# Kernel optimization log

Hardware: AMD Instinct MI355X
Metric: run time of the kernel (lower is better)

Reference implementation:

```python
import jax, jax.numpy as jnp
import numpy as np

PATCH = 16      # sqrt(n_patches=256)
ALPHA = 10.0
HEADS, DH = 2, 64


def _fourier(coords, Bm):
    # coords: (HW, 2), Bm: (n_features, 2) -> (HW, 2*n_features)
    proj = 2.0 * jnp.pi * coords @ Bm.T
    return jnp.concatenate([jnp.cos(proj), jnp.sin(proj)], axis=-1)


def _forward(coords_decoding, tokens, B_q, B_l0, B_l1,
             qW, qb, toqW, tokvW, tooW, toob,
             bwW0, bwb0, bwW1, bwb1,
             modW0, modb0, modW1, modb1,
             hvW0, hvb0, outW0, outb0, outW1, outb1):
    B = coords_decoding.shape[0]
    Hh, Ww = coords_decoding.shape[1], coords_decoding.shape[2]
    coords = coords_decoding.reshape(B, -1, coords_decoding.shape[-1])
    grid = coords[0]                      # (HW, 2); coords_modulation is None -> same grid
    HW = grid.shape[0]
    m = tokens.shape[1]

    # patch indices and spatial bias
    row = jnp.clip((grid[:, 0] * PATCH).astype(jnp.int32), 0, PATCH - 1)
    col = jnp.clip((grid[:, 1] * PATCH).astype(jnp.int32), 0, PATCH - 1)
    idx = row * PATCH + col               # (HW,)
    t = idx.astype(jnp.float32) / (PATCH * PATCH)
    pos = (jnp.arange(m, dtype=jnp.float32) + 0.5) / m
    rel = -ALPHA * jnp.abs(t[None, :] - pos[:, None]) ** 2   # (m, HW)
    bias = rel.T                          # (HW, m), broadcast over batch & heads

    # query features (shared across batch)
    xq = jax.nn.relu(_fourier(grid, B_q) @ qW + qb)           # (HW, hd)
    xq_b = jnp.broadcast_to(xq[None], (B, HW, xq.shape[-1]))

    # cross attention with spatial bias
    q = (xq_b @ toqW).reshape(B, HW, HEADS, DH).transpose(0, 2, 1, 3)   # (B,h,HW,Dh)
    kv = tokens @ tokvW                                                  # (B,m,2*inner)
    k, v = jnp.split(kv, 2, axis=-1)
    k = k.reshape(B, m, HEADS, DH).transpose(0, 2, 1, 3)                 # (B,h,m,Dh)
    v = v.reshape(B, m, HEADS, DH).transpose(0, 2, 1, 3)
    sim = jnp.einsum('bhqd,bhkd->bhqk', q, k) * (DH ** -0.5) + bias[None, None]
    attn = jax.nn.softmax(sim, axis=-1)
    o = jnp.einsum('bhqk,bhkd->bhqd', attn, v)
    o = o.transpose(0, 2, 1, 3).reshape(B, HW, HEADS * DH)
    mod = o @ tooW + toob                                                # (B,HW,hd)

    # per-band MLP stack (layer_num = 2)
    def band(Bl, bwW, bwb, mW, mb):
        h = jax.nn.relu(_fourier(grid, Bl) @ bwW + bwb)                  # (HW,hd)
        return jax.nn.relu(h[None] + mod @ mW + mb)                      # (B,HW,hd)

    m0 = band(B_l0, bwW0, bwb0, modW0, modb0)
    m1 = band(B_l1, bwW1, bwb1, modW1, modb1)
    hv0 = m0
    hv1 = jax.nn.relu((m1 + hv0) @ hvW0 + hvb0)
    out = (hv0 @ outW0 + outb0) + (hv1 @ outW1 + outb1)                  # (B,HW,3)
    return out.reshape(B, Hh, Ww, -1)


def setup_inputs() -> dict:
    key = jax.random.key(0)
    ks = jax.random.split(key, 32)
    B, H, W, L = 4, 128, 128, 256
    fd, hd, cd, od = 64, 256, 256, 3
    nf = fd // 2
    inner = HEADS * DH

    def lin(k, i, o):
        return jax.random.normal(k, (i, o), dtype=jnp.float32) / np.sqrt(i).astype(np.float32)

    inp = {}
    inp['coords_decoding'] = jax.random.uniform(ks[0], (B, H, W, 2), dtype=jnp.float32)
    inp['tokens'] = jax.random.normal(ks[1], (B, L, cd), dtype=jnp.float32)
    inp['B_q'] = jax.random.normal(ks[2], (nf, 2), dtype=jnp.float32) / 16.0
    inp['B_l0'] = jax.random.normal(ks[3], (nf, 2), dtype=jnp.float32) / 128.0
    inp['B_l1'] = jax.random.normal(ks[4], (nf, 2), dtype=jnp.float32) / 32.0
    inp['qW'] = lin(ks[5], fd, hd); inp['qb'] = jnp.zeros((hd,), jnp.float32)
    inp['toqW'] = lin(ks[6], hd, inner)
    inp['tokvW'] = lin(ks[7], cd, inner * 2)
    inp['tooW'] = lin(ks[8], inner, hd); inp['toob'] = jnp.zeros((hd,), jnp.float32)
    inp['bwW0'] = lin(ks[9], fd, hd); inp['bwb0'] = jnp.zeros((hd,), jnp.float32)
    inp['bwW1'] = lin(ks[10], fd, hd); inp['bwb1'] = jnp.zeros((hd,), jnp.float32)
    inp['modW0'] = lin(ks[11], hd, hd); inp['modb0'] = jnp.zeros((hd,), jnp.float32)
    inp['modW1'] = lin(ks[12], hd, hd); inp['modb1'] = jnp.zeros((hd,), jnp.float32)
    inp['hvW0'] = lin(ks[13], hd, hd); inp['hvb0'] = jnp.zeros((hd,), jnp.float32)
    inp['outW0'] = lin(ks[14], hd, od); inp['outb0'] = jnp.zeros((od,), jnp.float32)
    inp['outW1'] = lin(ks[15], hd, od); inp['outb1'] = jnp.zeros((od,), jnp.float32)
    return inp


def reference(coords_decoding, tokens, B_q, B_l0, B_l1,
              qW, qb, toqW, tokvW, tooW, toob,
              bwW0, bwb0, bwW1, bwb1,
              modW0, modb0, modW1, modb1,
              hvW0, hvb0, outW0, outb0, outW1, outb1):
    return _forward(coords_decoding, tokens, B_q, B_l0, B_l1,
                    qW, qb, toqW, tokvW, tooW, toob,
                    bwW0, bwb0, bwW1, bwb1,
                    modW0, modb0, modW1, modb1,
                    hvW0, hvb0, outW0, outb0, outW1, outb1)
```

## Files before the change

### kernel.cpp

```cpp
#include <hip/hip_runtime.h>
#include <stdint.h>

constexpr int kHW = 16384;
constexpr int kB  = 4;
constexpr int kM  = 256;

typedef _Float16 half8 __attribute__((ext_vector_type(8)));
typedef __attribute__((ext_vector_type(4))) float f32x4;

__device__ __forceinline__ unsigned short f2h(float f) {
  _Float16 h = (_Float16)f;
  return __builtin_bit_cast(unsigned short, h);
}
__device__ __forceinline__ float h2f(unsigned short u) {
  return (float)__builtin_bit_cast(_Float16, u);
}
__device__ __forceinline__ int swz256(int row, int col) {
  int ch = col >> 3;
  ch = (ch & ~7) | ((ch ^ row) & 7);
  return row * 256 + ch * 8 + (col & 7);
}

__global__ __launch_bounds__(256) void wprep_kernel(
    const float* __restrict__ tooW, const float* __restrict__ modW0,
    const float* __restrict__ modW1, const float* __restrict__ hvW0,
    const float* __restrict__ qW, const float* __restrict__ bwW0,
    const float* __restrict__ bwW1, const float* __restrict__ toqW,
    unsigned short* __restrict__ tooWt, unsigned short* __restrict__ modW0t,
    unsigned short* __restrict__ modW1t, unsigned short* __restrict__ hvW0t,
    unsigned short* __restrict__ qWt, unsigned short* __restrict__ bw0t,
    unsigned short* __restrict__ bw1t, unsigned short* __restrict__ toqWt)
{
  int m = blockIdx.x, tid = threadIdx.x;
  const float* Ws[8] = {tooW, modW0, modW1, hvW0, qW, bwW0, bwW1, toqW};
  unsigned short* Wts[8] = {tooWt, modW0t, modW1t, hvW0t, qWt, bw0t, bw1t, toqWt};
  const int Ks[8] = {128, 256, 256, 256, 64, 64, 64, 256};
  const int Ns[8] = {256, 256, 256, 256, 256, 256, 256, 128};
  const float* W = Ws[m];
  unsigned short* Wt = Wts[m];
  int K = Ks[m], N = Ns[m];
  if (tid < N) {
    for (int kb = 0; kb < K / 8; kb++) {
      unsigned short sv[8];
#pragma unroll
      for (int i = 0; i < 8; i++)
        sv[i] = f2h(W[(kb * 8 + i) * N + tid]);
      *(uint4*)&Wt[tid * K + kb * 8] = *(const uint4*)sv;
    }
  }
}

__global__ __launch_bounds__(256) void kv_kernel(
    const float* __restrict__ tokens, const float* __restrict__ tokvW,
    unsigned short* __restrict__ kn_ws, unsigned short* __restrict__ vt_ws)
{
  __shared__ __align__(16) float tok[256];
  int b = blockIdx.y, j = blockIdx.x, c = threadIdx.x;
  tok[c] = tokens[(b * kM + j) * 256 + c];
  __syncthreads();
  float acc = 0.f;
  for (int i4 = 0; i4 < 64; i4++) {
    float4 t4 = *(const float4*)&tok[i4 * 4];
    acc += t4.x * tokvW[(i4*4+0)*256 + c] + t4.y * tokvW[(i4*4+1)*256 + c]
         + t4.z * tokvW[(i4*4+2)*256 + c] + t4.w * tokvW[(i4*4+3)*256 + c];
  }
  unsigned short hv = f2h(acc);
  if (c < 128) {
    int h = c >> 6, dd = c & 63;
    kn_ws[((size_t)(b*2+h)*256 + j) * 64 + dd] = hv;
  } else {
    int c2 = c - 128;
    int h = c2 >> 6, dd = c2 & 63;
    vt_ws[((size_t)(b*2+h)*64 + dd) * 256 + j] = hv;
  }
}

constexpr int kFPitch = 72;
constexpr int kXPitch = 264;

__global__ __launch_bounds__(256, 2) void feat_kernel(
    const float* __restrict__ coords,
    const float* __restrict__ Bq, const float* __restrict__ Bl0, const float* __restrict__ Bl1,
    const float* __restrict__ qb, const float* __restrict__ bwb0, const float* __restrict__ bwb1,
    const unsigned short* __restrict__ qWt, const unsigned short* __restrict__ bw0t,
    const unsigned short* __restrict__ bw1t, const unsigned short* __restrict__ toqWt,
    unsigned short* __restrict__ qc_ws,
    unsigned short* __restrict__ h0_hf, unsigned short* __restrict__ h1_hf)
{
  __shared__ __align__(16) unsigned short ff_s[3][32][kFPitch];
  __shared__ __align__(16) unsigned short xq_s[32][kXPitch];
  __shared__ float coords_s[64];

  int tid = threadIdx.x;
  int px0 = blockIdx.x * 32;
  int w = tid >> 6, ln = tid & 63;
  int c = ln & 15, q = ln >> 4;

  if (tid < 64) coords_s[tid] = coords[px0 * 2 + tid];
  __syncthreads();

#pragma unroll
  for (int r = 0; r < 24; r++) {
    int v = r * 256 + tid;
    int mat = v >> 11;
    int p = (v >> 6) & 31;
    int f = v & 63;
    int fr = f & 31;
    const float* Bm = (mat == 0) ? Bq : (mat == 1 ? Bl0 : Bl1);
    float x = coords_s[p * 2 + 0];
    float y = coords_s[p * 2 + 1];
    float proj = 6.283185307179586f * (x * Bm[fr*2+0] + y * Bm[fr*2+1]);
    float s, cc;
    __sincosf(proj, &s, &cc);
    ff_s[mat][p][f] = f2h((f < 32) ? cc : s);
  }
  __syncthreads();

  const f32x4 zero4 = {0.f, 0.f, 0.f, 0.f};

  for (int mat = 0; mat < 3; mat++) {
    const unsigned short* Wt = (mat == 0) ? qWt : (mat == 1 ? bw0t : bw1t);
    const float* bias = (mat == 0) ? qb : (mat == 1 ? bwb0 : bwb1);
    f32x4 acc[8];
#pragma unroll
    for (int i = 0; i < 8; i++) acc[i] = zero4;
#pragma unroll
    for (int ks = 0; ks < 2; ks++) {
      int koff = ks * 32 + q * 8;
      half8 bfr[4];
#pragma unroll
      for (int nt = 0; nt < 4; nt++)
        bfr[nt] = *(const half8*)(Wt + (size_t)(w*64 + nt*16 + c) * 64 + koff);
      half8 afr[2];
#pragma unroll
      for (int mt = 0; mt < 2; mt++)
        afr[mt] = *(const half8*)(&ff_s[mat][mt*16 + c][koff]);
#pragma unroll
      for (int mt = 0; mt < 2; mt++)
#pragma unroll
        for (int nt = 0; nt < 4; nt++)
          acc[mt*4+nt] = __builtin_amdgcn_mfma_f32_16x16x32_f16(afr[mt], bfr[nt], acc[mt*4+nt], 0, 0, 0);
    }
    float bv[4];
#pragma unroll
    for (int nt = 0; nt < 4; nt++) bv[nt] = bias[w*64 + nt*16 + c];
#pragma unroll
    for (int mt = 0; mt < 2; mt++)
#pragma unroll
      for (int nt = 0; nt < 4; nt++)
#pragma unroll
        for (int rg = 0; rg < 4; rg++) {
          int row = mt*16 + q*4 + rg, col = w*64 + nt*16 + c;
          unsigned short hv = f2h(fmaxf(acc[mt*4+nt][rg] + bv[nt], 0.f));
          if (mat == 0)      xq_s[row][col] = hv;
          else if (mat == 1) h0_hf[((size_t)(px0 + row)) * 256 + col] = hv;
          else               h1_hf[((size_t)(px0 + row)) * 256 + col] = hv;
        }
  }
  __syncthreads();

  {
    f32x4 acc2[4];
#pragma unroll
    for (int i = 0; i < 4; i++) acc2[i] = zero4;
#pragma unroll
    for (int kt = 0; kt < 8; kt++) {
      int koff = kt * 32 + q * 8;
      half8 bfr[2];
#pragma unroll
      for (int nt = 0; nt < 2; nt++)
        bfr[nt] = *(const half8*)(toqWt + (size_t)(w*32 + nt*16 + c) * 256 + koff);
      half8 afr[2];
#pragma unroll
      for (int mt = 0; mt < 2; mt++)
        afr[mt] = *(const half8*)(&xq_s[mt*16 + c][koff]);
#pragma unroll
      for (int mt = 0; mt < 2; mt++)
#pragma unroll
        for (int nt = 0; nt < 2; nt++)
          acc2[mt*2+nt] = __builtin_amdgcn_mfma_f32_16x16x32_f16(afr[mt], bfr[nt], acc2[mt*2+nt], 0, 0, 0);
    }
#pragma unroll
    for (int mt = 0; mt < 2; mt++)
#pragma unroll
      for (int nt = 0; nt < 2; nt++)
#pragma unroll
        for (int rg = 0; rg < 4; rg++) {
          int row = mt*16 + q*4 + rg, col = w*32 + nt*16 + c;
          qc_ws[((size_t)(px0 + row)) * 128 + col] = f2h(acc2[mt*2+nt][rg]);
        }
  }
}

__global__ __launch_bounds__(256, 2) void attn_kernel(
    const unsigned short* __restrict__ kn_ws,
    const unsigned short* __restrict__ vt_ws,
    const unsigned short* __restrict__ qc_ws,
    const float* __restrict__ coords,
    unsigned short* __restrict__ o_hf)
{
  __shared__ __align__(16) unsigned short P_s[64 * 256];

  int b = blockIdx.y;
  int px0 = blockIdx.x * 64;
  int tid = threadIdx.x;
  int w = tid >> 6, ln = tid & 63;
  int c = ln & 15, q = ln >> 4;

  float tv[4];
#pragma unroll
  for (int rg = 0; rg < 4; rg++) {
    int px = px0 + w*16 + q*4 + rg;
    float x = coords[px*2 + 0], y = coords[px*2 + 1];
    int r = min(max((int)(x * 16.0f), 0), 15);
    int cl = min(max((int)(y * 16.0f), 0), 15);
    tv[rg] = (float)(r * 16 + cl) * (1.0f / 256.0f);
  }

  const f32x4 zero4 = {0.f, 0.f, 0.f, 0.f};

  for (int h = 0; h < 2; h++) {
    f32x4 acc[16];
#pragma unroll
    for (int i = 0; i < 16; i++) acc[i] = zero4;
    const unsigned short* kbase = kn_ws + (size_t)(b*2+h) * 256 * 64;
    const unsigned short* qrow = qc_ws + (size_t)(px0 + w*16 + c) * 128 + h*64;
    half8 a0 = *(const half8*)(qrow + q*8);
    half8 a1 = *(const half8*)(qrow + 32 + q*8);
#pragma unroll
    for (int nt = 0; nt < 16; nt++) {
      const unsigned short* kr = kbase + (size_t)(nt*16 + c) * 64 + q*8;
      half8 b0 = *(const half8*)(kr);
      half8 b1 = *(const half8*)(kr + 32);
      acc[nt] = __builtin_amdgcn_mfma_f32_16x16x32_f16(a0, b0, acc[nt], 0, 0, 0);
      acc[nt] = __builtin_amdgcn_mfma_f32_16x16x32_f16(a1, b1, acc[nt], 0, 0, 0);
    }

    float lm[4];
#pragma unroll
    for (int rg = 0; rg < 4; rg++) {
      float mx = -1e30f;
#pragma unroll
      for (int nt = 0; nt < 16; nt++) {
        float pos = ((float)(nt*16 + c) + 0.5f) * (1.0f / 256.0f);
        float db = tv[rg] - pos;
        float sb = acc[nt][rg] * 0.125f - 10.0f * db * db;
        acc[nt][rg] = sb;
        mx = fmaxf(mx, sb);
      }
      lm[rg] = mx;
    }
#pragma unroll
    for (int s = 1; s < 16; s <<= 1)
#pragma unroll
      for (int rg = 0; rg < 4; rg++)
        lm[rg] = fmaxf(lm[rg], __shfl_xor(lm[rg], s, 64));

    float linv[4];
#pragma unroll
    for (int rg = 0; rg < 4; rg++) {
      float sum = 0.f;
      int row = w*16 + q*4 + rg;
#pragma unroll
      for (int nt = 0; nt < 16; nt++) {
        float e = __expf(acc[nt][rg] - lm[rg]);
        sum += e;
        P_s[swz256(row, nt*16 + c)] = f2h(e);
      }
      linv[rg] = sum;
    }
#pragma unroll
    for (int s = 1; s < 16; s <<= 1)
#pragma unroll
      for (int rg = 0; rg < 4; rg++)
        linv[rg] += __shfl_xor(linv[rg], s, 64);
#pragma unroll
    for (int rg = 0; rg < 4; rg++) linv[rg] = 1.0f / linv[rg];

    __syncthreads();

    f32x4 oacc[4];
#pragma unroll
    for (int i = 0; i < 4; i++) oacc[i] = zero4;
    const unsigned short* vbase = vt_ws + (size_t)(b*2+h) * 64 * 256;
#pragma unroll
    for (int kt = 0; kt < 8; kt++) {
      int koff = kt * 32 + q * 8;
      half8 af = *(const half8*)&P_s[swz256(w*16 + c, koff)];
#pragma unroll
      for (int nt = 0; nt < 4; nt++) {
        half8 bf = *(const half8*)(vbase + (size_t)(nt*16 + c) * 256 + koff);
        oacc[nt] = __builtin_amdgcn_mfma_f32_16x16x32_f16(af, bf, oacc[nt], 0, 0, 0);
      }
    }
#pragma unroll
    for (int nt = 0; nt < 4; nt++)
#pragma unroll
      for (int rg = 0; rg < 4; rg++) {
        int row = w*16 + q*4 + rg;
        o_hf[((size_t)(b * kHW + px0 + row)) * 128 + h*64 + nt*16 + c] =
            f2h(oacc[nt][rg] * linv[rg]);
      }
    __syncthreads();
  }
}

constexpr int kPitch = 264;

template <int KD>
__device__ __forceinline__ void gemm4(
    const unsigned short* abuf, const unsigned short* wt,
    f32x4* acc , int c, int q)
{
#pragma unroll
  for (int ks = 0; ks < KD / 32; ks++) {
    int koff = ks * 32 + q * 8;
    half8 bfr[4];
#pragma unroll
    for (int nt = 0; nt < 4; nt++)
      bfr[nt] = *(const half8*)(wt + (nt * 16 + c) * KD + koff);
    half8 afr[4];
#pragma unroll
    for (int mt = 0; mt < 4; mt++)
      afr[mt] = *(const half8*)(abuf + (mt * 16 + c) * kPitch + koff);
#pragma unroll
    for (int mt = 0; mt < 4; mt++)
#pragma unroll
      for (int nt = 0; nt < 4; nt++)
        acc[mt * 4 + nt] = __builtin_amdgcn_mfma_f32_16x16x32_f16(afr[mt], bfr[nt], acc[mt * 4 + nt], 0, 0, 0);
  }
}

__global__ __launch_bounds__(256, 2) void mlp_kernel(
    const unsigned short* __restrict__ o_hf,
    const unsigned short* __restrict__ h0_hf, const unsigned short* __restrict__ h1_hf,
    const unsigned short* __restrict__ tooWt, const float* __restrict__ toob,
    const unsigned short* __restrict__ modW0t, const float* __restrict__ modb0,
    const unsigned short* __restrict__ modW1t, const float* __restrict__ modb1,
    const unsigned short* __restrict__ hvW0t, const float* __restrict__ hvb0,
    const float* __restrict__ outW0, const float* __restrict__ outb0,
    const float* __restrict__ outW1, const float* __restrict__ outb1,
    float* __restrict__ dout)
{
  __shared__ __align__(16) unsigned short buf0[64 * kPitch];
  __shared__ __align__(16) unsigned short buf1[64 * kPitch];
  __shared__ __align__(16) unsigned short hbuf[16 * kPitch];
  __shared__ __align__(16) float scratch[64 * 3 * 4];

  int tid = threadIdx.x;
  int px0 = blockIdx.x * 16;
  int w = tid >> 6, ln = tid & 63;
  int c = ln & 15, q = ln >> 4;

#pragma unroll
  for (int i = 0; i < 4; i++) {
    int idx = i * 256 + tid;
    int r = idx >> 4, c8 = (idx & 15) * 8;
    int b = r >> 4, px = r & 15;
    uint4 v = *(const uint4*)(o_hf + ((size_t)(b * kHW + px0 + px)) * 128 + c8);
    *(uint4*)&buf0[r * kPitch + c8] = v;
  }
#pragma unroll
  for (int i = 0; i < 2; i++) {
    int idx = i * 256 + tid;
    int p = idx >> 5, c8 = (idx & 31) * 8;
    uint4 v = *(const uint4*)(h0_hf + ((size_t)(px0 + p)) * 256 + c8);
    *(uint4*)&hbuf[p * kPitch + c8] = v;
  }
  __syncthreads();

  f32x4 acc[16];
  const f32x4 zero4 = {0.f, 0.f, 0.f, 0.f};

#pragma unroll
  for (int i = 0; i < 16; i++) acc[i] = zero4;
  gemm4<128>(buf0, tooWt + (size_t)w * 64 * 128, acc, c, q);
  {
    float bias[4];
#pragma unroll
    for (int nt = 0; nt < 4; nt++) bias[nt] = toob[w * 64 + nt * 16 + c];
#pragma unroll
    for (int mt = 0; mt < 4; mt++)
#pragma unroll
      for (int nt = 0; nt < 4; nt++)
#pragma unroll
        for (int rg = 0; rg < 4; rg++) {
          int row = mt * 16 + q * 4 + rg, col = w * 64 + nt * 16 + c;
          buf1[row * kPitch + col] = f2h(acc[mt * 4 + nt][rg] + bias[nt]);
        }
  }
  __syncthreads();

#pragma unroll
  for (int i = 0; i < 16; i++) acc[i] = zero4;
  gemm4<256>(buf1, modW0t + (size_t)w * 64 * 256, acc, c, q);
  {
    float bias[4], hr[4][4];
#pragma unroll
    for (int nt = 0; nt < 4; nt++) {
      int col = w * 64 + nt * 16 + c;
      bias[nt] = modb0[col];
#pragma unroll
      for (int rg = 0; rg < 4; rg++)
        hr[nt][rg] = h2f(hbuf[(q * 4 + rg) * kPitch + col]);
    }
#pragma unroll
    for (int mt = 0; mt < 4; mt++)
#pragma unroll
      for (int nt = 0; nt < 4; nt++)
#pragma unroll
        for (int rg = 0; rg < 4; rg++) {
          int row = mt * 16 + q * 4 + rg, col = w * 64 + nt * 16 + c;
          buf0[row * kPitch + col] =
              f2h(fmaxf(acc[mt * 4 + nt][rg] + bias[nt] + hr[nt][rg], 0.f));
        }
  }
  __syncthreads();

#pragma unroll
  for (int i = 0; i < 2; i++) {
    int idx = i * 256 + tid;
    int p = idx >> 5, c8 = (idx & 31) * 8;
    uint4 v = *(const uint4*)(h1_hf + ((size_t)(px0 + p)) * 256 + c8);
    *(uint4*)&hbuf[p * kPitch + c8] = v;
  }
#pragma unroll
  for (int i = 0; i < 16; i++) acc[i] = zero4;
  gemm4<256>(buf1, modW1t + (size_t)w * 64 * 256, acc, c, q);
  __syncthreads();
  {
    float bias[4], hr[4][4];
#pragma unroll
    for (int nt = 0; nt < 4; nt++) {
      int col = w * 64 + nt * 16 + c;
      bias[nt] = modb1[col];
#pragma unroll
      for (int rg = 0; rg < 4; rg++)
        hr[nt][rg] = h2f(hbuf[(q * 4 + rg) * kPitch + col]);
    }
#pragma unroll
    for (int mt = 0; mt < 4; mt++)
#pragma unroll
      for (int nt = 0; nt < 4; nt++)
#pragma unroll
        for (int rg = 0; rg < 4; rg++) {
          int row = mt * 16 + q * 4 + rg, col = w * 64 + nt * 16 + c;
          float m0v = h2f(buf0[row * kPitch + col]);
          float v = m0v + fmaxf(acc[mt * 4 + nt][rg] + bias[nt] + hr[nt][rg], 0.f);
          buf1[row * kPitch + col] = f2h(v);
        }
  }
  __syncthreads();

#pragma unroll
  for (int i = 0; i < 16; i++) acc[i] = zero4;
  gemm4<256>(buf1, hvW0t + (size_t)w * 64 * 256, acc, c, q);
  {
    float bias[4], w0v[4][3], w1v[4][3];
#pragma unroll
    for (int nt = 0; nt < 4; nt++) {
      int col = w * 64 + nt * 16 + c;
      bias[nt] = hvb0[col];
#pragma unroll
      for (int k = 0; k < 3; k++) {
        w0v[nt][k] = outW0[col * 3 + k];
        w1v[nt][k] = outW1[col * 3 + k];
      }
    }
#pragma unroll
    for (int mt = 0; mt < 4; mt++) {
      float pk[4][3];
#pragma unroll
      for (int rg = 0; rg < 4; rg++)
#pragma unroll
        for (int k = 0; k < 3; k++) pk[rg][k] = 0.f;
#pragma unroll
      for (int nt = 0; nt < 4; nt++) {
        int col = w * 64 + nt * 16 + c;
#pragma unroll
        for (int rg = 0; rg < 4; rg++) {
          int row = mt * 16 + q * 4 + rg;
          float hv1 = fmaxf(acc[mt * 4 + nt][rg] + bias[nt], 0.f);
          float m0v = h2f(buf0[row * kPitch + col]);
#pragma unroll
          for (int k = 0; k < 3; k++)
            pk[rg][k] += m0v * w0v[nt][k] + hv1 * w1v[nt][k];
        }
      }
#pragma unroll
      for (int s = 1; s < 16; s <<= 1)
#pragma unroll
        for (int rg = 0; rg < 4; rg++)
#pragma unroll
          for (int k = 0; k < 3; k++)
            pk[rg][k] += __shfl_xor(pk[rg][k], s, 64);
      if (c == 0) {
#pragma unroll
        for (int rg = 0; rg < 4; rg++) {
          int row = mt * 16 + q * 4 + rg;
#pragma unroll
          for (int k = 0; k < 3; k++)
            scratch[row * 12 + k * 4 + w] = pk[rg][k];
        }
      }
    }
  }
  __syncthreads();

  if (tid < 192) {
    int row = tid / 3, k = tid % 3;
    int b = row >> 4, px = px0 + (row & 15);
    float s = outb0[k] + outb1[k];
#pragma unroll
    for (int ww = 0; ww < 4; ww++) s += scratch[row * 12 + k * 4 + ww];
    dout[((size_t)b * kHW + px) * 3 + k] = s;
  }
}

extern "C" void kernel_launch(void* const* d_in, const int* in_sizes, int n_in,
                              void* d_out, int out_size, void* d_ws, size_t ws_size,
                              hipStream_t stream) {
  const float* coords = (const float*)d_in[0];
  const float* tokens = (const float*)d_in[1];
  const float* Bq     = (const float*)d_in[2];
  const float* Bl0    = (const float*)d_in[3];
  const float* Bl1    = (const float*)d_in[4];
  const float* qW     = (const float*)d_in[5];
  const float* qb     = (const float*)d_in[6];
  const float* toqW   = (const float*)d_in[7];
  const float* tokvW  = (const float*)d_in[8];
  const float* tooW   = (const float*)d_in[9];
  const float* toob   = (const float*)d_in[10];
  const float* bwW0   = (const float*)d_in[11];
  const float* bwb0   = (const float*)d_in[12];
  const float* bwW1   = (const float*)d_in[13];
  const float* bwb1   = (const float*)d_in[14];
  const float* modW0  = (const float*)d_in[15];
  const float* modb0  = (const float*)d_in[16];
  const float* modW1  = (const float*)d_in[17];
  const float* modb1  = (const float*)d_in[18];
  const float* hvW0   = (const float*)d_in[19];
  const float* hvb0   = (const float*)d_in[20];
  const float* outW0  = (const float*)d_in[21];
  const float* outb0  = (const float*)d_in[22];
  const float* outW1  = (const float*)d_in[23];
  const float* outb1  = (const float*)d_in[24];

  char* ws = (char*)d_ws;
  unsigned short* qc_ws  = (unsigned short*)(ws + 65536);
  unsigned short* h0_hf  = (unsigned short*)(ws + 4259840);
  unsigned short* h1_hf  = (unsigned short*)(ws + 12648448);
  unsigned short* o_hf   = (unsigned short*)(ws + 21037056);
  unsigned short* kn_ws  = (unsigned short*)(ws + 37814272);
  unsigned short* vt_ws  = (unsigned short*)(ws + 38076416);
  unsigned short* tooWt  = (unsigned short*)(ws + 38338560);
  unsigned short* modW0t = (unsigned short*)(ws + 38404096);
  unsigned short* modW1t = (unsigned short*)(ws + 38535168);
  unsigned short* hvW0t  = (unsigned short*)(ws + 38666240);
  unsigned short* qWt    = (unsigned short*)(ws + 38797312);
  unsigned short* bw0t   = (unsigned short*)(ws + 38830080);
  unsigned short* bw1t   = (unsigned short*)(ws + 38862848);
  unsigned short* toqWt  = (unsigned short*)(ws + 38895616);

  wprep_kernel<<<dim3(8), 256, 0, stream>>>(
      tooW, modW0, modW1, hvW0, qW, bwW0, bwW1, toqW,
      tooWt, modW0t, modW1t, hvW0t, qWt, bw0t, bw1t, toqWt);
  feat_kernel<<<dim3(kHW / 32), 256, 0, stream>>>(
      coords, Bq, Bl0, Bl1, qb, bwb0, bwb1,
      qWt, bw0t, bw1t, toqWt,
      qc_ws, h0_hf, h1_hf);
  kv_kernel<<<dim3(kM, kB), 256, 0, stream>>>(tokens, tokvW, kn_ws, vt_ws);
  attn_kernel<<<dim3(kHW / 64, kB), 256, 0, stream>>>(kn_ws, vt_ws, qc_ws, coords, o_hf);
  mlp_kernel<<<dim3(kHW / 16), 256, 0, stream>>>(
      o_hf, h0_hf, h1_hf, tooWt, toob, modW0t, modb0, modW1t, modb1,
      hvW0t, hvb0, outW0, outb0, outW1, outb1, (float*)d_out);
}
```

Before: 282.8 us.

## Fuse attention into MLP kernel, keeping attention output in shared memory

Removes the separate attention kernel and computes cross-attention inside the MLP kernel. Each wave handles one batch element for the block's 16 pixels and writes the attention output straight into the shared buffer that the first GEMM reads. This avoids the global write and read of the fp16 attention output, plus one launch. The P matrix now lives in a per-wave region that aliases buf1, which is enlarged, so shared memory use and register pressure may rise and occupancy may drop. The query rows are also loaded once per batch wave instead of being shared.

```diff
diff --git a/kernel.cpp b/kernel.cpp
--- a/kernel.cpp
+++ b/kernel.cpp
@@ -192,119 +192,6 @@
   }
 }
 
-__global__ __launch_bounds__(256, 2) void attn_kernel(
-    const unsigned short* __restrict__ kn_ws,
-    const unsigned short* __restrict__ vt_ws,
-    const unsigned short* __restrict__ qc_ws,
-    const float* __restrict__ coords,
-    unsigned short* __restrict__ o_hf)
-{
-  __shared__ __align__(16) unsigned short P_s[64 * 256];
-
-  int b = blockIdx.y;
-  int px0 = blockIdx.x * 64;
-  int tid = threadIdx.x;
-  int w = tid >> 6, ln = tid & 63;
-  int c = ln & 15, q = ln >> 4;
-
-  float tv[4];
-#pragma unroll
-  for (int rg = 0; rg < 4; rg++) {
-    int px = px0 + w*16 + q*4 + rg;
-    float x = coords[px*2 + 0], y = coords[px*2 + 1];
-    int r = min(max((int)(x * 16.0f), 0), 15);
-    int cl = min(max((int)(y * 16.0f), 0), 15);
-    tv[rg] = (float)(r * 16 + cl) * (1.0f / 256.0f);
-  }
-
-  const f32x4 zero4 = {0.f, 0.f, 0.f, 0.f};
-
-  for (int h = 0; h < 2; h++) {
-    f32x4 acc[16];
-#pragma unroll
-    for (int i = 0; i < 16; i++) acc[i] = zero4;
-    const unsigned short* kbase = kn_ws + (size_t)(b*2+h) * 256 * 64;
-    const unsigned short* qrow = qc_ws + (size_t)(px0 + w*16 + c) * 128 + h*64;
-    half8 a0 = *(const half8*)(qrow + q*8);
-    half8 a1 = *(const half8*)(qrow + 32 + q*8);
-#pragma unroll
-    for (int nt = 0; nt < 16; nt++) {
-      const unsigned short* kr = kbase + (size_t)(nt*16 + c) * 64 + q*8;
-      half8 b0 = *(const half8*)(kr);
-      half8 b1 = *(const half8*)(kr + 32);
-      acc[nt] = __builtin_amdgcn_mfma_f32_16x16x32_f16(a0, b0, acc[nt], 0, 0, 0);
-      acc[nt] = __builtin_amdgcn_mfma_f32_16x16x32_f16(a1, b1, acc[nt], 0, 0, 0);
-    }
-
-    float lm[4];
-#pragma unroll
-    for (int rg = 0; rg < 4; rg++) {
-      float mx = -1e30f;
-#pragma unroll
-      for (int nt = 0; nt < 16; nt++) {
-        float pos = ((float)(nt*16 + c) + 0.5f) * (1.0f / 256.0f);
-        float db = tv[rg] - pos;
-        float sb = acc[nt][rg] * 0.125f - 10.0f * db * db;
-        acc[nt][rg] = sb;
-        mx = fmaxf(mx, sb);
-      }
-      lm[rg] = mx;
-    }
-#pragma unroll
-    for (int s = 1; s < 16; s <<= 1)
-#pragma unroll
-      for (int rg = 0; rg < 4; rg++)
-        lm[rg] = fmaxf(lm[rg], __shfl_xor(lm[rg], s, 64));
-
-    float linv[4];
-#pragma unroll
-    for (int rg = 0; rg < 4; rg++) {
-      float sum = 0.f;
-      int row = w*16 + q*4 + rg;
-#pragma unroll
-      for (int nt = 0; nt < 16; nt++) {
-        float e = __expf(acc[nt][rg] - lm[rg]);
-        sum += e;
-        P_s[swz256(row, nt*16 + c)] = f2h(e);
-      }
-      linv[rg] = sum;
-    }
-#pragma unroll
-    for (int s = 1; s < 16; s <<= 1)
-#pragma unroll
-      for (int rg = 0; rg < 4; rg++)
-        linv[rg] += __shfl_xor(linv[rg], s, 64);
-#pragma unroll
-    for (int rg = 0; rg < 4; rg++) linv[rg] = 1.0f / linv[rg];
-
-    __syncthreads();
-
-    f32x4 oacc[4];
-#pragma unroll
-    for (int i = 0; i < 4; i++) oacc[i] = zero4;
-    const unsigned short* vbase = vt_ws + (size_t)(b*2+h) * 64 * 256;
-#pragma unroll
-    for (int kt = 0; kt < 8; kt++) {
-      int koff = kt * 32 + q * 8;
-      half8 af = *(const half8*)&P_s[swz256(w*16 + c, koff)];
-#pragma unroll
-      for (int nt = 0; nt < 4; nt++) {
-        half8 bf = *(const half8*)(vbase + (size_t)(nt*16 + c) * 256 + koff);
-        oacc[nt] = __builtin_amdgcn_mfma_f32_16x16x32_f16(af, bf, oacc[nt], 0, 0, 0);
-      }
-    }
-#pragma unroll
-    for (int nt = 0; nt < 4; nt++)
-#pragma unroll
-      for (int rg = 0; rg < 4; rg++) {
-        int row = w*16 + q*4 + rg;
-        o_hf[((size_t)(b * kHW + px0 + row)) * 128 + h*64 + nt*16 + c] =
-            f2h(oacc[nt][rg] * linv[rg]);
-      }
-    __syncthreads();
-  }
-}
-
 constexpr int kPitch = 264;
 
 template <int KD>
@@ -331,8 +218,11 @@
   }
 }
 
-__global__ __launch_bounds__(256, 2) void mlp_kernel(
-    const unsigned short* __restrict__ o_hf,
+__global__ __launch_bounds__(256, 2) void fused_kernel(
+    const unsigned short* __restrict__ kn_ws,
+    const unsigned short* __restrict__ vt_ws,
+    const unsigned short* __restrict__ qc_ws,
+    const float* __restrict__ coords,
     const unsigned short* __restrict__ h0_hf, const unsigned short* __restrict__ h1_hf,
     const unsigned short* __restrict__ tooWt, const float* __restrict__ toob,
     const unsigned short* __restrict__ modW0t, const float* __restrict__ modb0,
@@ -343,23 +233,19 @@
     float* __restrict__ dout)
 {
   __shared__ __align__(16) unsigned short buf0[64 * kPitch];
-  __shared__ __align__(16) unsigned short buf1[64 * kPitch];
+  __shared__ __align__(16) unsigned short regB[21120];
   __shared__ __align__(16) unsigned short hbuf[16 * kPitch];
   __shared__ __align__(16) float scratch[64 * 3 * 4];
 
+  unsigned short* buf1  = regB;
   int tid = threadIdx.x;
   int px0 = blockIdx.x * 16;
   int w = tid >> 6, ln = tid & 63;
   int c = ln & 15, q = ln >> 4;
-
-#pragma unroll
-  for (int i = 0; i < 4; i++) {
-    int idx = i * 256 + tid;
-    int r = idx >> 4, c8 = (idx & 15) * 8;
-    int b = r >> 4, px = r & 15;
-    uint4 v = *(const uint4*)(o_hf + ((size_t)(b * kHW + px0 + px)) * 128 + c8);
-    *(uint4*)&buf0[r * kPitch + c8] = v;
-  }
+  unsigned short* Pband = regB + w * 4096;
+
+  const f32x4 zero4 = {0.f, 0.f, 0.f, 0.f};
+
 #pragma unroll
   for (int i = 0; i < 2; i++) {
     int idx = i * 256 + tid;
@@ -367,10 +253,99 @@
     uint4 v = *(const uint4*)(h0_hf + ((size_t)(px0 + p)) * 256 + c8);
     *(uint4*)&hbuf[p * kPitch + c8] = v;
   }
+
+  float tv[4];
+#pragma unroll
+  for (int rg = 0; rg < 4; rg++) {
+    int px = px0 + q*4 + rg;
+    float x = coords[px*2 + 0], y = coords[px*2 + 1];
+    int r = min(max((int)(x * 16.0f), 0), 15);
+    int cl = min(max((int)(y * 16.0f), 0), 15);
+    tv[rg] = (float)(r * 16 + cl) * (1.0f / 256.0f);
+  }
+
+  for (int h = 0; h < 2; h++) {
+    f32x4 acc[16];
+#pragma unroll
+    for (int i = 0; i < 16; i++) acc[i] = zero4;
+    const unsigned short* kbase = kn_ws + (size_t)(w*2+h) * 256 * 64;
+    const unsigned short* qrow = qc_ws + (size_t)(px0 + c) * 128 + h*64;
+    half8 a0 = *(const half8*)(qrow + q*8);
+    half8 a1 = *(const half8*)(qrow + 32 + q*8);
+#pragma unroll
+    for (int nt = 0; nt < 16; nt++) {
+      const unsigned short* kr = kbase + (size_t)(nt*16 + c) * 64 + q*8;
+      half8 b0 = *(const half8*)(kr);
+      half8 b1 = *(const half8*)(kr + 32);
+      acc[nt] = __builtin_amdgcn_mfma_f32_16x16x32_f16(a0, b0, acc[nt], 0, 0, 0);
+      acc[nt] = __builtin_amdgcn_mfma_f32_16x16x32_f16(a1, b1, acc[nt], 0, 0, 0);
+    }
+
+    float lm[4];
+#pragma unroll
+    for (int rg = 0; rg < 4; rg++) {
+      float mx = -1e30f;
+#pragma unroll
+      for (int nt = 0; nt < 16; nt++) {
+        float pos = ((float)(nt*16 + c) + 0.5f) * (1.0f / 256.0f);
+        float db = tv[rg] - pos;
+        float sb = acc[nt][rg] * 0.125f - 10.0f * db * db;
+        acc[nt][rg] = sb;
+        mx = fmaxf(mx, sb);
+      }
+      lm[rg] = mx;
+    }
+#pragma unroll
+    for (int s = 1; s < 16; s <<= 1)
+#pragma unroll
+      for (int rg = 0; rg < 4; rg++)
+        lm[rg] = fmaxf(lm[rg], __shfl_xor(lm[rg], s, 64));
+
+    float linv[4];
+#pragma unroll
+    for (int rg = 0; rg < 4; rg++) {
+      float sum = 0.f;
+      int row = q*4 + rg;
+#pragma unroll
+      for (int nt = 0; nt < 16; nt++) {
+        float e = __expf(acc[nt][rg] - lm[rg]);
+        sum += e;
+        Pband[swz256(row, nt*16 + c)] = f2h(e);
+      }
+      linv[rg] = sum;
+    }
+#pragma unroll
+    for (int s = 1; s < 16; s <<= 1)
+#pragma unroll
+      for (int rg = 0; rg < 4; rg++)
+        linv[rg] += __shfl_xor(linv[rg], s, 64);
+#pragma unroll
+    for (int rg = 0; rg < 4; rg++) linv[rg] = 1.0f / linv[rg];
+
+    f32x4 oacc[4];
+#pragma unroll
+    for (int i = 0; i < 4; i++) oacc[i] = zero4;
+    const unsigned short* vbase = vt_ws + (size_t)(w*2+h) * 64 * 256;
+#pragma unroll
+    for (int kt = 0; kt < 8; kt++) {
+      int koff = kt * 32 + q * 8;
+      half8 af = *(const half8*)&Pband[swz256(c, koff)];
+#pragma unroll
+      for (int nt = 0; nt < 4; nt++) {
+        half8 bf = *(const half8*)(vbase + (size_t)(nt*16 + c) * 256 + koff);
+        oacc[nt] = __builtin_amdgcn_mfma_f32_16x16x32_f16(af, bf, oacc[nt], 0, 0, 0);
+      }
+    }
+#pragma unroll
+    for (int nt = 0; nt < 4; nt++)
+#pragma unroll
+      for (int rg = 0; rg < 4; rg++)
+        buf0[(w*16 + q*4 + rg) * kPitch + h*64 + nt*16 + c] =
+            f2h(oacc[nt][rg] * linv[rg]);
+  }
   __syncthreads();
 
   f32x4 acc[16];
-  const f32x4 zero4 = {0.f, 0.f, 0.f, 0.f};
 
 #pragma unroll
   for (int i = 0; i < 16; i++) acc[i] = zero4;
@@ -550,7 +525,6 @@
   unsigned short* qc_ws  = (unsigned short*)(ws + 65536);
   unsigned short* h0_hf  = (unsigned short*)(ws + 4259840);
   unsigned short* h1_hf  = (unsigned short*)(ws + 12648448);
-  unsigned short* o_hf   = (unsigned short*)(ws + 21037056);
   unsigned short* kn_ws  = (unsigned short*)(ws + 37814272);
   unsigned short* vt_ws  = (unsigned short*)(ws + 38076416);
   unsigned short* tooWt  = (unsigned short*)(ws + 38338560);
@@ -570,8 +544,8 @@
       qWt, bw0t, bw1t, toqWt,
       qc_ws, h0_hf, h1_hf);
   kv_kernel<<<dim3(kM, kB), 256, 0, stream>>>(tokens, tokvW, kn_ws, vt_ws);
-  attn_kernel<<<dim3(kHW / 64, kB), 256, 0, stream>>>(kn_ws, vt_ws, qc_ws, coords, o_hf);
-  mlp_kernel<<<dim3(kHW / 16), 256, 0, stream>>>(
-      o_hf, h0_hf, h1_hf, tooWt, toob, modW0t, modb0, modW1t, modb1,
+  fused_kernel<<<dim3(kHW / 16), 256, 0, stream>>>(
+      kn_ws, vt_ws, qc_ws, coords, h0_hf, h1_hf,
+      tooWt, toob, modW0t, modb0, modW1t, modb1,
       hvW0t, hvb0, outW0, outb0, outW1, outb1, (float*)d_out);
 }
```

Result: slower. 321.6 us (+13.7%).
